# Kernel tuning notes

Hardware: AMD Instinct MI355X
Metric: run time of the kernel (lower is better)

Reference implementation:

```python
import jax, jax.numpy as jnp
import numpy as np
from jax import lax

K = 3
K2 = K * K
EPS = 1e-5


def conv3x3(x, w, b=None):
    # x [B,C,H,W], w [O,C,3,3], padding=1, stride=1
    out = lax.conv_general_dilated(x, w, (1, 1), [(1, 1), (1, 1)],
                                   dimension_numbers=('NCHW', 'OIHW', 'NCHW'))
    if b is not None:
        out = out + b[None, :, None, None]
    return out


def deform_conv(x, w_off, b_off, w_mod, b_mod, w):
    # DCNv2-style deformable conv, k=3, stride=1, pad=1, dilation=1, no bias.
    B, C, H, W = x.shape
    O = w.shape[0]
    off = conv3x3(x, w_off, b_off).reshape(B, K2, 2, H, W)   # (dy,dx) per tap
    mod = 2.0 * jax.nn.sigmoid(conv3x3(x, w_mod, b_mod))      # [B,9,H,W]
    dy, dx = off[:, :, 0], off[:, :, 1]

    ky = (jnp.arange(K) - 1).astype(x.dtype)
    base_y = jnp.repeat(ky, K)   # [9]
    base_x = jnp.tile(ky, K)     # [9]
    ii = jnp.arange(H, dtype=x.dtype)[:, None]
    jj = jnp.arange(W, dtype=x.dtype)[None, :]
    py = ii[None, None] + base_y[None, :, None, None] + dy   # [B,9,H,W]
    px = jj[None, None] + base_x[None, :, None, None] + dx

    def sample(xb, pyb, pxb):
        # xb [C,H,W]; pyb/pxb [9,H,W] -> [C,9,H,W], bilinear w/ zero pad
        y0 = jnp.floor(pyb)
        x0 = jnp.floor(pxb)
        wy = pyb - y0
        wx = pxb - x0
        flat = xb.reshape(C, -1)
        acc = jnp.zeros((C, K2, H, W), xb.dtype)
        for yc, xc, wt in ((y0, x0, (1 - wy) * (1 - wx)),
                           (y0, x0 + 1, (1 - wy) * wx),
                           (y0 + 1, x0, wy * (1 - wx)),
                           (y0 + 1, x0 + 1, wy * wx)):
            yi = yc.astype(jnp.int32)
            xi = xc.astype(jnp.int32)
            valid = (yi >= 0) & (yi < H) & (xi >= 0) & (xi < W)
            idx = (jnp.clip(yi, 0, H - 1) * W + jnp.clip(xi, 0, W - 1)).reshape(-1)
            g = jnp.take(flat, idx, axis=1).reshape(C, K2, H, W)
            acc = acc + g * (wt * valid)[None]
        return acc

    patches = jax.vmap(sample)(x, py, px)          # [B,C,9,H,W]
    patches = patches * mod[:, None]               # modulated
    return jnp.einsum('bckhw,ock->bohw', patches, w.reshape(O, C, K2))


def bn_relu(x):
    # BatchNorm2d(affine=False), train-mode batch stats, biased variance
    mean = jnp.mean(x, axis=(0, 2, 3), keepdims=True)
    var = jnp.mean(jnp.square(x - mean), axis=(0, 2, 3), keepdims=True)
    return jax.nn.relu((x - mean) * lax.rsqrt(var + EPS))


def maxpool2(x):
    return lax.reduce_window(x, -jnp.inf, lax.max, (1, 1, 2, 2), (1, 1, 2, 2), 'VALID')


def setup_inputs() -> dict:
    key = jax.random.key(0)
    ks = jax.random.split(key, 11)
    B, Cin, Cout, H, W = 4, 64, 128, 128, 128
    std1 = 1.0 / np.sqrt(Cin * K2)
    std2 = 1.0 / np.sqrt(Cout * K2)
    return {
        'x': jax.random.normal(ks[0], (B, Cin, H, W), jnp.float32),
        'w_off1': jax.random.normal(ks[1], (2 * K2, Cin, K, K), jnp.float32) * 0.01,
        'b_off1': jax.random.normal(ks[2], (2 * K2,), jnp.float32) * 0.01,
        'w_mod1': jax.random.normal(ks[3], (K2, Cin, K, K), jnp.float32) * 0.01,
        'b_mod1': jnp.zeros((K2,), jnp.float32),
        'w1': jax.random.normal(ks[4], (Cout, Cin, K, K), jnp.float32) * std1,
        'w_off2': jax.random.normal(ks[5], (2 * K2, Cout, K, K), jnp.float32) * 0.01,
        'b_off2': jax.random.normal(ks[6], (2 * K2,), jnp.float32) * 0.01,
        'w_mod2': jax.random.normal(ks[7], (K2, Cout, K, K), jnp.float32) * 0.01,
        'b_mod2': jnp.zeros((K2,), jnp.float32),
        'w2': jax.random.normal(ks[8], (Cout, Cout, K, K), jnp.float32) * std2,
    }


def reference(x, w_off1, b_off1, w_mod1, b_mod1, w1,
              w_off2, b_off2, w_mod2, b_mod2, w2):
    h = bn_relu(deform_conv(x, w_off1, b_off1, w_mod1, b_mod1, w1))
    h = bn_relu(deform_conv(h, w_off2, b_off2, w_mod2, b_mod2, w2))
    return maxpool2(h)
```

## Files before the change

### kernel.cpp

```cpp
#include <hip/hip_runtime.h>
#include <math.h>

#define HH 128
#define WW 128
#define HWSZ 16384

typedef __attribute__((ext_vector_type(8))) _Float16 h8;
typedef __attribute__((ext_vector_type(2))) _Float16 h2;
typedef __attribute__((ext_vector_type(4))) float f32x4;
typedef __attribute__((ext_vector_type(2))) float f32x2;
typedef unsigned short ushort;

__device__ __forceinline__ ushort f2h(float f) {
    _Float16 h = (_Float16)f;
    ushort u;
    __builtin_memcpy(&u, &h, 2);
    return u;
}
__device__ __forceinline__ unsigned f2h2(float lo, float hi) {
    h2 r;
    r.x = (_Float16)lo;
    r.y = (_Float16)hi;
    unsigned u;
    __builtin_memcpy(&u, &r, 4);
    return u;
}
__device__ __forceinline__ f32x2 unpk_h2(unsigned u) {
    h2 h;
    __builtin_memcpy(&h, &u, 4);
    return (f32x2){(float)h.x, (float)h.y};
}

__global__ __launch_bounds__(256) void prep_weights(
    const float* __restrict__ w1, const float* __restrict__ w2,
    const float* __restrict__ w_off1, const float* __restrict__ w_mod1,
    const float* __restrict__ w_off2, const float* __restrict__ w_mod2,
    ushort* __restrict__ Wt1, ushort* __restrict__ Wt2,
    ushort* __restrict__ Wo1, ushort* __restrict__ Wo2) {
    int bid = blockIdx.x, tid = threadIdx.x;
    if (bid < 336) {
        int i = bid * 256 + tid;
        int o = i / 672, kq = i % 672;
        int k = kq / 72, c = kq % 72;
        float v = (k < 9 && c < 64) ? w1[(o * 64 + c) * 9 + k] : 0.f;
        Wt1[i] = f2h(v);
    } else if (bid < 960) {
        int i = (bid - 336) * 256 + tid;
        int o = i / 1248, kq = i % 1248;
        int k = kq / 136, c = kq % 136;
        float v = (k < 9 && c < 128) ? w2[(o * 128 + c) * 9 + k] : 0.f;
        Wt2[i] = f2h(v);
    } else if (bid < 1032) {
        int i = (bid - 960) * 256 + tid;
        int o = i / 576, kap = i % 576;
        int k = kap / 64, c = kap % 64;
        float v = 0.f;
        if (o < 18) v = w_off1[(o * 64 + c) * 9 + k];
        else if (o < 27) v = w_mod1[((o - 18) * 64 + c) * 9 + k];
        Wo1[i] = f2h(v);
    } else {
        int i = (bid - 1032) * 256 + tid;
        int o = i / 1152, kap = i % 1152;
        int k = kap / 128, c = kap % 128;
        float v = 0.f;
        if (o < 18) v = w_off2[(o * 128 + c) * 9 + k];
        else if (o < 27) v = w_mod2[((o - 18) * 128 + c) * 9 + k];
        Wo2[i] = f2h(v);
    }
}

template <int C>
__global__ __launch_bounds__(256) void nhwc_cvt(const float* __restrict__ xin,
                                                unsigned* __restrict__ xout) {
    __shared__ float tile[64][C + 1];
    const int m0 = blockIdx.x * 64;
    const int b = m0 >> 14;
    const int hw0 = m0 & 16383;
    const int t = threadIdx.x;
    const int pr = t & 63, cr = t >> 6;
#pragma unroll
    for (int it = 0; it < C / 4; ++it) {
        int c = it * 4 + cr;
        tile[pr][c] = xin[(((size_t)(b * C + c)) << 14) + hw0 + pr];
    }
    __syncthreads();
    constexpr int CH = C / 2;
#pragma unroll
    for (int it = 0; it < 64 * CH / 256; ++it) {
        int slot = it * 256 + t;
        int p = slot / CH, cc = slot % CH;
        xout[(size_t)(m0 + p) * CH + cc] =
            f2h2(tile[p][2 * cc], tile[p][2 * cc + 1]);
    }
}

__global__ __launch_bounds__(256) void bn_apply_ew(
    const unsigned* __restrict__ xin, const float* __restrict__ praw,
    unsigned* __restrict__ xout) {
    __shared__ float lstats[256];
    if (threadIdx.x < 128) {
        int c = threadIdx.x;
        float s = 0.f, q = 0.f;
#pragma unroll
        for (int r = 0; r < 8; ++r) {
            s += praw[r * 256 + c];
            q += praw[r * 256 + 128 + c];
        }
        float mean = s / 65536.f;
        float var = q / 65536.f - mean * mean;
        lstats[c] = mean;
        lstats[128 + c] = rsqrtf(var + 1e-5f);
    }
    __syncthreads();
    int i = blockIdx.x * 256 + threadIdx.x;
    uint4 v = ((const uint4*)xin)[i];
    int c0 = ((i * 4) & 63) * 2;
    unsigned ov[4];
    unsigned in[4] = {v.x, v.y, v.z, v.w};
#pragma unroll
    for (int d = 0; d < 4; ++d) {
        int c = c0 + 2 * d;
        f32x2 f = unpk_h2(in[d]);
        float a = fmaxf(0.f, (f.x - lstats[c]) * lstats[128 + c]);
        float b2 = fmaxf(0.f, (f.y - lstats[c + 1]) * lstats[128 + c + 1]);
        ov[d] = f2h2(a, b2);
    }
    ((uint4*)xout)[i] = uint4{ov[0], ov[1], ov[2], ov[3]};
}

template <int C>
__global__ __launch_bounds__(256) void offmod_nhwc(
    const ushort* __restrict__ xh, const ushort* __restrict__ wt,
    const float* __restrict__ b_off, const float* __restrict__ b_mod,
    float* __restrict__ dyb, float* __restrict__ dxb, float* __restrict__ mob,
    float* __restrict__ praw) {
    constexpr int K = C * 9;
    if (blockIdx.x < 8) praw[blockIdx.x * 256 + threadIdx.x] = 0.f;
    const int m0 = blockIdx.x * 64;
    const int b = m0 >> 14;
    const int hw0 = m0 & 16383;
    const int h = hw0 >> 7;
    const int w0 = hw0 & 127;
    const int tid = threadIdx.x;
    const int lane = tid & 63, wv = tid >> 6;
    const int n16 = lane & 15, quad = lane >> 4;
    const int p = wv * 16 + n16;
    const int w = w0 + p;

    int tbase[9];
    bool tval[9];
#pragma unroll
    for (int k = 0; k < 9; ++k) {
        int yy = h + k / 3 - 1, xx = w + k % 3 - 1;
        tval[k] = ((unsigned)yy < 128u) && ((unsigned)xx < 128u);
        int cy = min(max(yy, 0), 127), cx = min(max(xx, 0), 127);
        tbase[k] = ((b << 14) + (cy << 7) + cx) * C + quad * 8;
    }

    f32x4 acc[2];
    acc[0] = (f32x4){0.f, 0.f, 0.f, 0.f};
    acc[1] = (f32x4){0.f, 0.f, 0.f, 0.f};

    const ushort* b0p = wt + (size_t)n16 * K + quad * 8;
    const ushort* b1p = wt + (size_t)(16 + n16) * K + quad * 8;

#pragma unroll
    for (int s = 0; s < K / 32; ++s) {
        const int k = (s * 32) / C;
        const int c0 = (s * 32) % C;
        h8 a = {0, 0, 0, 0, 0, 0, 0, 0};
        if (tval[k]) a = *(const h8*)(xh + (size_t)tbase[k] + c0);
        const h8 bv0 = *(const h8*)(b0p + s * 32);
        const h8 bv1 = *(const h8*)(b1p + s * 32);
        acc[0] = __builtin_amdgcn_mfma_f32_16x16x32_f16(a, bv0, acc[0], 0, 0, 0);
        acc[1] = __builtin_amdgcn_mfma_f32_16x16x32_f16(a, bv1, acc[1], 0, 0, 0);
    }

    __shared__ float sm[32 * 65];
#pragma unroll
    for (int nt = 0; nt < 2; ++nt) {
        int n = nt * 16 + n16;
        int pb = wv * 16 + quad * 4;
#pragma unroll
        for (int r = 0; r < 4; ++r) sm[n * 65 + pb + r] = acc[nt][r];
    }
    __syncthreads();
    {
        int n = tid >> 3, i8 = tid & 7;
        if (n < 27) {
            const float* sp = sm + n * 65 + i8 * 8;
            int px = hw0 + i8 * 8;
            if (n < 18) {
                int k = n >> 1;
                float bias = b_off[n];
                float* dst =
                    ((n & 1) ? dxb : dyb) + (((size_t)(b * 9 + k)) << 14) + px;
#pragma unroll
                for (int j = 0; j < 8; j += 4) {
                    float4 v = make_float4(sp[j] + bias, sp[j + 1] + bias,
                                           sp[j + 2] + bias, sp[j + 3] + bias);
                    *(float4*)(dst + j) = v;
                }
            } else {
                float bias = b_mod[n - 18];
                float* dst = mob + (((size_t)(b * 9 + (n - 18))) << 14) + px;
#pragma unroll
                for (int j = 0; j < 8; j += 4) {
                    float4 v;
                    v.x = 2.f / (1.f + expf(-(sp[j] + bias)));
                    v.y = 2.f / (1.f + expf(-(sp[j + 1] + bias)));
                    v.z = 2.f / (1.f + expf(-(sp[j + 2] + bias)));
                    v.w = 2.f / (1.f + expf(-(sp[j + 3] + bias)));
                    *(float4*)(dst + j) = v;
                }
            }
        }
    }
}

template <int C>
__global__ __launch_bounds__(256, 8) void deform_mfma3(
    const ushort* __restrict__ xh, const float* __restrict__ dyb,
    const float* __restrict__ dxb, const float* __restrict__ mob,
    const ushort* __restrict__ wt, unsigned* __restrict__ xout,
    float* __restrict__ praw) {
    constexpr int PIX = 32;
    constexpr int NCH = C / 8;
    constexpr int NCC = C / 8;
    constexpr int NIT = PIX * NCC / 256;
    constexpr int HNIT = (NIT >= 2) ? NIT / 2 : 1;
    constexpr int SH = (C / 32) / 2 > 0 ? (C / 32) / 2 : 1;
    constexpr int CPW = C + 8;
    constexpr int KP = ((9 * CPW + 31) / 32) * 32;
    constexpr int ABUF = PIX * C;
    constexpr int LOOPB = 2 * ABUF * 2 + PIX * 9 * 4 + PIX * 9 * 8;
    constexpr int EPIB = 128 * (PIX + 1) * 4;
    constexpr int SMEMB = LOOPB > EPIB ? LOOPB : EPIB;

    __shared__ __align__(16) char smem_raw[SMEMB];
    ushort* abuf0 = (ushort*)smem_raw;
    ushort* abuf1 = abuf0 + ABUF;
    int* tbl = (int*)(abuf0 + 2 * ABUF);
    unsigned* twl = (unsigned*)(smem_raw + 2 * ABUF * 2 + PIX * 9 * 4);

    const int bid = (blockIdx.x & 7) * (gridDim.x >> 3) + (blockIdx.x >> 3);
    const int m0 = bid * PIX;
    const int b = m0 >> 14;
    const int hw0 = m0 & 16383;
    const int h = hw0 >> 7, w0 = hw0 & 127;
    const int tid = threadIdx.x;
    const int lane = tid & 63, wv = tid >> 6;
    const int n16 = lane & 15, quad = lane >> 4;
    const int xr = n16 & (NCH - 1);

    for (int r = tid; r < PIX * 9; r += 256) {
        int p = r & (PIX - 1), k = r >> 5;
        int oi = ((b * 9 + k) << 14) + hw0 + p;
        float py = (float)(h + k / 3 - 1) + dyb[oi];
        float px = (float)(w0 + p + k % 3 - 1) + dxb[oi];
        float mv = mob[oi];
        float y0f = floorf(py), x0f = floorf(px);
        float wy = py - y0f, wx = px - x0f;
        int y0 = (int)y0f, x0 = (int)x0f;
        int y1 = y0 + 1, x1 = x0 + 1;
        float f00 = (1.f - wy) * (1.f - wx) *
                    (((unsigned)y0 < 128u && (unsigned)x0 < 128u) ? mv : 0.f);
        float f01 = (1.f - wy) * wx *
                    (((unsigned)y0 < 128u && (unsigned)x1 < 128u) ? mv : 0.f);
        float f10 = wy * (1.f - wx) *
                    (((unsigned)y1 < 128u && (unsigned)x0 < 128u) ? mv : 0.f);
        float f11 = wy * wx *
                    (((unsigned)y1 < 128u && (unsigned)x1 < 128u) ? mv : 0.f);
        int cy0 = min(max(y0, 0), 127), cy1 = min(max(y1, 0), 127);
        int cx0 = min(max(x0, 0), 127), cx1 = min(max(x1, 0), 127);
        int base00 = (((b << 14) + (cy0 << 7) + cx0)) * C;
        int flags = ((cy1 != cy0) ? 2 : 0) | ((cx1 != cx0) ? 1 : 0);
        int s = p * 9 + k;
        tbl[s] = base00 | flags;
        twl[2 * s] = f2h2(f00, f01);
        twl[2 * s + 1] = f2h2(f10, f11);
    }
    __syncthreads();

    auto issue_loads = [&](int kc, int it0, uint4 (&q)[HNIT][4],
                           uint2 (&fw)[HNIT]) {
#pragma unroll
        for (int j = 0; j < HNIT; ++j) {
            int e = (it0 + j) * 256 + tid;
            int p = e / NCC, cc = e % NCC;
            int s = p * 9 + kc;
            int ent = tbl[s];
            fw[j] = *(const uint2*)&twl[2 * s];
            int base = ent & ~3;
            int dxo = (ent & 1) ? C : 0;
            int dyo = (ent & 2) ? (C << 7) : 0;
            const ushort* pp = xh + (size_t)base + cc * 8;
            q[j][0] = *(const uint4*)(pp);
            q[j][1] = *(const uint4*)(pp + dxo);
            q[j][2] = *(const uint4*)(pp + dyo);
            q[j][3] = *(const uint4*)(pp + dyo + dxo);
        }
    };
    auto interp_write = [&](ushort* dst, int it0, uint4 (&q)[HNIT][4],
                            uint2 (&fw)[HNIT]) {
#pragma unroll
        for (int j = 0; j < HNIT; ++j) {
            int e = (it0 + j) * 256 + tid;
            int p = e / NCC, cc = e % NCC;
            h2 w01, w23;
            __builtin_memcpy(&w01, &fw[j].x, 4);
            __builtin_memcpy(&w23, &fw[j].y, 4);
            h8 F0 = {w01.x, w01.x, w01.x, w01.x, w01.x, w01.x, w01.x, w01.x};
            h8 F1 = {w01.y, w01.y, w01.y, w01.y, w01.y, w01.y, w01.y, w01.y};
            h8 F2 = {w23.x, w23.x, w23.x, w23.x, w23.x, w23.x, w23.x, w23.x};
            h8 F3 = {w23.y, w23.y, w23.y, w23.y, w23.y, w23.y, w23.y, w23.y};
            h8 a0, a1, a2, a3;
            __builtin_memcpy(&a0, &q[j][0], 16);
            __builtin_memcpy(&a1, &q[j][1], 16);
            __builtin_memcpy(&a2, &q[j][2], 16);
            __builtin_memcpy(&a3, &q[j][3], 16);
            h8 v = a0 * F0 + a1 * F1 + a2 * F2 + a3 * F3;
            uint4 ov;
            __builtin_memcpy(&ov, &v, 16);
            int ccs = cc ^ (p & (NCH - 1));
            *(uint4*)&dst[p * C + ccs * 8] = ov;
        }
    };

    f32x4 acc[2][2];
#pragma unroll
    for (int mt = 0; mt < 2; ++mt)
#pragma unroll
        for (int nt = 0; nt < 2; ++nt) acc[mt][nt] = (f32x4){0.f, 0.f, 0.f, 0.f};

    const ushort* bbase[2];
#pragma unroll
    for (int nt = 0; nt < 2; ++nt)
        bbase[nt] = wt + (size_t)(wv * 32 + nt * 16 + n16) * KP + quad * 8;

    auto mfma_run = [&](const ushort* ab, int kc, int s0, int s1) {
#pragma unroll
        for (int s = s0; s < s1; ++s) {
            h8 av[2], bv[2];
            int ch = (s * 4 + quad) ^ xr;
#pragma unroll
            for (int mt = 0; mt < 2; ++mt)
                av[mt] = *(const h8*)(ab + (mt * 16 + n16) * C + ch * 8);
#pragma unroll
            for (int nt = 0; nt < 2; ++nt)
                bv[nt] = *(const h8*)(bbase[nt] + kc * CPW + s * 32);
#pragma unroll
            for (int mt = 0; mt < 2; ++mt)
#pragma unroll
                for (int nt = 0; nt < 2; ++nt)
                    acc[mt][nt] = __builtin_amdgcn_mfma_f32_16x16x32_f16(
                        av[mt], bv[nt], acc[mt][nt], 0, 0, 0);
        }
    };

    {
        uint4 q[HNIT][4];
        uint2 fw[HNIT];
        issue_loads(0, 0, q, fw);
        interp_write(abuf0, 0, q, fw);
        if constexpr (NIT >= 2) {
            issue_loads(0, HNIT, q, fw);
            interp_write(abuf0, HNIT, q, fw);
        }
    }
    __syncthreads();

#pragma unroll 1
    for (int kc = 0; kc < 9; ++kc) {
        const ushort* ab = (kc & 1) ? abuf1 : abuf0;
        ushort* dst = (kc & 1) ? abuf0 : abuf1;
        uint4 q[HNIT][4];
        uint2 fw[HNIT];
        if (kc < 8) issue_loads(kc + 1, 0, q, fw);
        __builtin_amdgcn_s_setprio(1);
        mfma_run(ab, kc, 0, SH);
        __builtin_amdgcn_s_setprio(0);
        if constexpr (NIT >= 2) {
            if (kc < 8) {
                interp_write(dst, 0, q, fw);
                issue_loads(kc + 1, HNIT, q, fw);
            }
            __builtin_amdgcn_s_setprio(1);
            mfma_run(ab, kc, SH, C / 32);
            __builtin_amdgcn_s_setprio(0);
            if (kc < 8) interp_write(dst, HNIT, q, fw);
        } else {
            __builtin_amdgcn_s_setprio(1);
            mfma_run(ab, kc, SH, C / 32);
            __builtin_amdgcn_s_setprio(0);
            if (kc < 8) interp_write(dst, 0, q, fw);
        }
        __syncthreads();
    }

    float* sm = (float*)smem_raw;
    constexpr int SROW = PIX + 1;
#pragma unroll
    for (int mt = 0; mt < 2; ++mt)
#pragma unroll
        for (int nt = 0; nt < 2; ++nt) {
            int o = wv * 32 + nt * 16 + n16;
            int mb = mt * 16 + quad * 4;
#pragma unroll
            for (int r = 0; r < 4; ++r) sm[o * SROW + mb + r] = acc[mt][nt][r];
        }
    __syncthreads();
    {
        int o = tid >> 1, half = tid & 1;
        const float* sp = sm + o * SROW + half * 16;
        float s = 0.f, qq = 0.f;
#pragma unroll
        for (int i = 0; i < 16; i += 4) {
            float4 v = make_float4(sp[i], sp[i + 1], sp[i + 2], sp[i + 3]);
            s += v.x + v.y + v.z + v.w;
            qq += v.x * v.x + v.y * v.y + v.z * v.z + v.w * v.w;
        }
        s += __shfl_down(s, 1, 64);
        qq += __shfl_down(qq, 1, 64);
        if (half == 0) {
            float* pr = praw + (blockIdx.x & 7) * 256;
            atomicAdd(&pr[o], s);
            atomicAdd(&pr[128 + o], qq);
        }
    }
    {
        int p = tid >> 3, cc8 = tid & 7;
        unsigned ov[8];
#pragma unroll
        for (int j = 0; j < 8; ++j) {
            int c = cc8 * 16 + 2 * j;
            ov[j] = f2h2(sm[c * SROW + p], sm[(c + 1) * SROW + p]);
        }
        uint4* dst = (uint4*)(xout + ((size_t)(m0 + p)) * 64 + cc8 * 8);
        dst[0] = uint4{ov[0], ov[1], ov[2], ov[3]};
        dst[1] = uint4{ov[4], ov[5], ov[6], ov[7]};
    }
}

template <int C>
__global__ __launch_bounds__(256, 8) void deform_mfma3p(
    const ushort* __restrict__ xh, const float* __restrict__ dyb,
    const float* __restrict__ dxb, const float* __restrict__ mob,
    const ushort* __restrict__ wt, float* __restrict__ pout,
    float* __restrict__ praw) {
    constexpr int PIX = 32;
    constexpr int NCH = C / 8;
    constexpr int NCC = C / 8;
    constexpr int NIT = PIX * NCC / 256;
    constexpr int HNIT = (NIT >= 2) ? NIT / 2 : 1;
    constexpr int SH = (C / 32) / 2 > 0 ? (C / 32) / 2 : 1;
    constexpr int CPW = C + 8;
    constexpr int KP = ((9 * CPW + 31) / 32) * 32;
    constexpr int ABUF = PIX * C;
    constexpr int LOOPB = 2 * ABUF * 2 + PIX * 9 * 4 + PIX * 9 * 8;
    constexpr int EPIB = 128 * (PIX + 1) * 4;
    constexpr int SMEMB = LOOPB > EPIB ? LOOPB : EPIB;

    __shared__ __align__(16) char smem_raw[SMEMB];
    ushort* abuf0 = (ushort*)smem_raw;
    ushort* abuf1 = abuf0 + ABUF;
    int* tbl = (int*)(abuf0 + 2 * ABUF);
    unsigned* twl = (unsigned*)(smem_raw + 2 * ABUF * 2 + PIX * 9 * 4);

    const int bid = (blockIdx.x & 7) * (gridDim.x >> 3) + (blockIdx.x >> 3);
    const int b = bid >> 9;
    const int rp = (bid >> 3) & 63;
    const int g = bid & 7;
    const int tid = threadIdx.x;
    const int lane = tid & 63, wv = tid >> 6;
    const int n16 = lane & 15, quad = lane >> 4;
    const int xr = n16 & (NCH - 1);

    for (int r = tid; r < PIX * 9; r += 256) {
        int p = r & (PIX - 1), k = r >> 5;
        int row = 2 * rp + (p >> 4), col = g * 16 + (p & 15);
        int oi = ((b * 9 + k) << 14) + (row << 7) + col;
        float py = (float)(row + k / 3 - 1) + dyb[oi];
        float px = (float)(col + k % 3 - 1) + dxb[oi];
        float mv = mob[oi];
        float y0f = floorf(py), x0f = floorf(px);
        float wy = py - y0f, wx = px - x0f;
        int y0 = (int)y0f, x0 = (int)x0f;
        int y1 = y0 + 1, x1 = x0 + 1;
        float f00 = (1.f - wy) * (1.f - wx) *
                    (((unsigned)y0 < 128u && (unsigned)x0 < 128u) ? mv : 0.f);
        float f01 = (1.f - wy) * wx *
                    (((unsigned)y0 < 128u && (unsigned)x1 < 128u) ? mv : 0.f);
        float f10 = wy * (1.f - wx) *
                    (((unsigned)y1 < 128u && (unsigned)x0 < 128u) ? mv : 0.f);
        float f11 = wy * wx *
                    (((unsigned)y1 < 128u && (unsigned)x1 < 128u) ? mv : 0.f);
        int cy0 = min(max(y0, 0), 127), cy1 = min(max(y1, 0), 127);
        int cx0 = min(max(x0, 0), 127), cx1 = min(max(x1, 0), 127);
        int base00 = (((b << 14) + (cy0 << 7) + cx0)) * C;
        int flags = ((cy1 != cy0) ? 2 : 0) | ((cx1 != cx0) ? 1 : 0);
        int s = p * 9 + k;
        tbl[s] = base00 | flags;
        twl[2 * s] = f2h2(f00, f01);
        twl[2 * s + 1] = f2h2(f10, f11);
    }
    __syncthreads();

    auto issue_loads = [&](int kc, int it0, uint4 (&q)[HNIT][4],
                           uint2 (&fw)[HNIT]) {
#pragma unroll
        for (int j = 0; j < HNIT; ++j) {
            int e = (it0 + j) * 256 + tid;
            int p = e / NCC, cc = e % NCC;
            int s = p * 9 + kc;
            int ent = tbl[s];
            fw[j] = *(const uint2*)&twl[2 * s];
            int base = ent & ~3;
            int dxo = (ent & 1) ? C : 0;
            int dyo = (ent & 2) ? (C << 7) : 0;
            const ushort* pp = xh + (size_t)base + cc * 8;
            q[j][0] = *(const uint4*)(pp);
            q[j][1] = *(const uint4*)(pp + dxo);
            q[j][2] = *(const uint4*)(pp + dyo);
            q[j][3] = *(const uint4*)(pp + dyo + dxo);
        }
    };
    auto interp_write = [&](ushort* dst, int it0, uint4 (&q)[HNIT][4],
                            uint2 (&fw)[HNIT]) {
#pragma unroll
        for (int j = 0; j < HNIT; ++j) {
            int e = (it0 + j) * 256 + tid;
            int p = e / NCC, cc = e % NCC;
            h2 w01, w23;
            __builtin_memcpy(&w01, &fw[j].x, 4);
            __builtin_memcpy(&w23, &fw[j].y, 4);
            h8 F0 = {w01.x, w01.x, w01.x, w01.x, w01.x, w01.x, w01.x, w01.x};
            h8 F1 = {w01.y, w01.y, w01.y, w01.y, w01.y, w01.y, w01.y, w01.y};
            h8 F2 = {w23.x, w23.x, w23.x, w23.x, w23.x, w23.x, w23.x, w23.x};
            h8 F3 = {w23.y, w23.y, w23.y, w23.y, w23.y, w23.y, w23.y, w23.y};
            h8 a0, a1, a2, a3;
            __builtin_memcpy(&a0, &q[j][0], 16);
            __builtin_memcpy(&a1, &q[j][1], 16);
            __builtin_memcpy(&a2, &q[j][2], 16);
            __builtin_memcpy(&a3, &q[j][3], 16);
            h8 v = a0 * F0 + a1 * F1 + a2 * F2 + a3 * F3;
            uint4 ov;
            __builtin_memcpy(&ov, &v, 16);
            int ccs = cc ^ (p & (NCH - 1));
            *(uint4*)&dst[p * C + ccs * 8] = ov;
        }
    };

    f32x4 acc[2][2];
#pragma unroll
    for (int mt = 0; mt < 2; ++mt)
#pragma unroll
        for (int nt = 0; nt < 2; ++nt) acc[mt][nt] = (f32x4){0.f, 0.f, 0.f, 0.f};

    const ushort* bbase[2];
#pragma unroll
    for (int nt = 0; nt < 2; ++nt)
        bbase[nt] = wt + (size_t)(wv * 32 + nt * 16 + n16) * KP + quad * 8;

    auto mfma_run = [&](const ushort* ab, int kc, int s0, int s1) {
#pragma unroll
        for (int s = s0; s < s1; ++s) {
            h8 av[2], bv[2];
            int ch = (s * 4 + quad) ^ xr;
#pragma unroll
            for (int mt = 0; mt < 2; ++mt)
                av[mt] = *(const h8*)(ab + (mt * 16 + n16) * C + ch * 8);
#pragma unroll
            for (int nt = 0; nt < 2; ++nt)
                bv[nt] = *(const h8*)(bbase[nt] + kc * CPW + s * 32);
#pragma unroll
            for (int mt = 0; mt < 2; ++mt)
#pragma unroll
                for (int nt = 0; nt < 2; ++nt)
                    acc[mt][nt] = __builtin_amdgcn_mfma_f32_16x16x32_f16(
                        av[mt], bv[nt], acc[mt][nt], 0, 0, 0);
        }
    };

    {
        uint4 q[HNIT][4];
        uint2 fw[HNIT];
        issue_loads(0, 0, q, fw);
        interp_write(abuf0, 0, q, fw);
        if constexpr (NIT >= 2) {
            issue_loads(0, HNIT, q, fw);
            interp_write(abuf0, HNIT, q, fw);
        }
    }
    __syncthreads();

#pragma unroll 1
    for (int kc = 0; kc < 9; ++kc) {
        const ushort* ab = (kc & 1) ? abuf1 : abuf0;
        ushort* dst = (kc & 1) ? abuf0 : abuf1;
        uint4 q[HNIT][4];
        uint2 fw[HNIT];
        if (kc < 8) issue_loads(kc + 1, 0, q, fw);
        __builtin_amdgcn_s_setprio(1);
        mfma_run(ab, kc, 0, SH);
        __builtin_amdgcn_s_setprio(0);
        if constexpr (NIT >= 2) {
            if (kc < 8) {
                interp_write(dst, 0, q, fw);
                issue_loads(kc + 1, HNIT, q, fw);
            }
            __builtin_amdgcn_s_setprio(1);
            mfma_run(ab, kc, SH, C / 32);
            __builtin_amdgcn_s_setprio(0);
            if (kc < 8) interp_write(dst, HNIT, q, fw);
        } else {
            __builtin_amdgcn_s_setprio(1);
            mfma_run(ab, kc, SH, C / 32);
            __builtin_amdgcn_s_setprio(0);
            if (kc < 8) interp_write(dst, 0, q, fw);
        }
        __syncthreads();
    }

    float* sm = (float*)smem_raw;
    constexpr int SROW = PIX + 1;
#pragma unroll
    for (int mt = 0; mt < 2; ++mt)
#pragma unroll
        for (int nt = 0; nt < 2; ++nt) {
            int o = wv * 32 + nt * 16 + n16;
            int mb = mt * 16 + quad * 4;
#pragma unroll
            for (int r = 0; r < 4; ++r) sm[o * SROW + mb + r] = acc[mt][nt][r];
        }
    __syncthreads();
    {
        int o = tid >> 1, half = tid & 1;
        const float* so = sm + o * SROW;
        const float* sp = so + half * 16;
        float s = 0.f, qq = 0.f;
#pragma unroll
        for (int i = 0; i < 16; i += 4) {
            float4 v = make_float4(sp[i], sp[i + 1], sp[i + 2], sp[i + 3]);
            s += v.x + v.y + v.z + v.w;
            qq += v.x * v.x + v.y * v.y + v.z * v.z + v.w * v.w;
        }
        s += __shfl_down(s, 1, 64);
        qq += __shfl_down(qq, 1, 64);
        if (half == 0) {
            float* pr = praw + (blockIdx.x & 7) * 256;
            atomicAdd(&pr[o], s);
            atomicAdd(&pr[128 + o], qq);
        }
        float4 pv;
#pragma unroll
        for (int i = 0; i < 4; ++i) {
            int pc = half * 4 + i;
            float m0v = fmaxf(so[2 * pc], so[2 * pc + 1]);
            float m1v = fmaxf(so[16 + 2 * pc], so[16 + 2 * pc + 1]);
            ((float*)&pv)[i] = fmaxf(m0v, m1v);
        }
        *(float4*)(pout + (((size_t)(b * 128 + o)) << 12) + rp * 64 + g * 8 +
                   half * 4) = pv;
    }
}

__global__ __launch_bounds__(256) void pool_norm(const float* __restrict__ pout,
                                                 const float* __restrict__ praw,
                                                 float* __restrict__ out) {
    __shared__ float lstats[256];
    if (threadIdx.x < 128) {
        int c = threadIdx.x;
        float s = 0.f, q = 0.f;
#pragma unroll
        for (int r = 0; r < 8; ++r) {
            s += praw[r * 256 + c];
            q += praw[r * 256 + 128 + c];
        }
        float mean = s / 65536.f;
        float var = q / 65536.f - mean * mean;
        lstats[c] = mean;
        lstats[128 + c] = rsqrtf(var + 1e-5f);
    }
    __syncthreads();
    int i = blockIdx.x * 256 + threadIdx.x;
    int c = (i >> 10) & 127;
    float mean = lstats[c], rstd = lstats[128 + c];
    float4 v = ((const float4*)pout)[i];
    v.x = fmaxf(0.f, (v.x - mean) * rstd);
    v.y = fmaxf(0.f, (v.y - mean) * rstd);
    v.z = fmaxf(0.f, (v.z - mean) * rstd);
    v.w = fmaxf(0.f, (v.w - mean) * rstd);
    ((float4*)out)[i] = v;
}

extern "C" void kernel_launch(void* const* d_in, const int* in_sizes, int n_in,
                              void* d_out, int out_size, void* d_ws,
                              size_t ws_size, hipStream_t stream) {
    (void)in_sizes;
    (void)n_in;
    (void)out_size;
    (void)ws_size;
    const float* x = (const float*)d_in[0];
    const float* w_off1 = (const float*)d_in[1];
    const float* b_off1 = (const float*)d_in[2];
    const float* w_mod1 = (const float*)d_in[3];
    const float* b_mod1 = (const float*)d_in[4];
    const float* w1 = (const float*)d_in[5];
    const float* w_off2 = (const float*)d_in[6];
    const float* b_off2 = (const float*)d_in[7];
    const float* w_mod2 = (const float*)d_in[8];
    const float* b_mod2 = (const float*)d_in[9];
    const float* w2 = (const float*)d_in[10];
    float* out = (float*)d_out;
    float* ws = (float*)d_ws;

    ushort* Wt1 = (ushort*)ws;
    ushort* Wt2 = (ushort*)(ws + 43008);
    ushort* Wo1 = (ushort*)(ws + 43008 + 79872);
    ushort* Wo2 = (ushort*)(ws + 43008 + 79872 + 16384);
    float* dyb = ws + 172032;
    float* dxb = dyb + 589824;
    float* mob = dxb + 589824;
    float* hbuf = mob + 589824;
    float* xhf = hbuf + 8388608;
    float* h1hf = xhf + 2097152;
    float* praw = h1hf + 4194304;
    ushort* xh = (ushort*)xhf;
    ushort* h1h = (ushort*)h1hf;

    prep_weights<<<1176, 256, 0, stream>>>(w1, w2, w_off1, w_mod1, w_off2,
                                           w_mod2, Wt1, Wt2, Wo1, Wo2);

    nhwc_cvt<64><<<1024, 256, 0, stream>>>(x, (unsigned*)xh);
    offmod_nhwc<64><<<1024, 256, 0, stream>>>(xh, Wo1, b_off1, b_mod1, dyb, dxb,
                                              mob, praw);
    deform_mfma3<64><<<2048, 256, 0, stream>>>(xh, dyb, dxb, mob, Wt1,
                                               (unsigned*)hbuf, praw);
    bn_apply_ew<<<4096, 256, 0, stream>>>((const unsigned*)hbuf, praw,
                                          (unsigned*)h1h);

    offmod_nhwc<128><<<1024, 256, 0, stream>>>(h1h, Wo2, b_off2, b_mod2, dyb,
                                               dxb, mob, praw);
    deform_mfma3p<128><<<2048, 256, 0, stream>>>(h1h, dyb, dxb, mob, Wt2, hbuf,
                                                 praw);
    pool_norm<<<2048, 256, 0, stream>>>(hbuf, praw, out);
}
```

Before: 299.4 us.

## Compute BN stats and maxpool from MFMA registers, drop LDS epilogue staging

The final deformable-conv kernel no longer stages the accumulator tile through shared memory for its epilogue. The per-channel sum and sum-of-squares come from registers with cross-lane xor shuffles, and the 2x2 maxpool is taken directly from the MFMA output layout. This removes an LDS round trip and a barrier and shrinks the shared-memory footprint to the main-loop buffers. The launch-bounds occupancy hint on both deform kernels is also lowered from 8 to 6, giving the compiler more registers at some cost in waves per CU; pooled outputs are now written as scalar stores rather than float4.

```diff
diff --git a/kernel.cpp b/kernel.cpp
--- a/kernel.cpp
+++ b/kernel.cpp
@@ -219,7 +219,7 @@
 }
 
 template <int C>
-__global__ __launch_bounds__(256, 8) void deform_mfma3(
+__global__ __launch_bounds__(256, 6) void deform_mfma3(
     const ushort* __restrict__ xh, const float* __restrict__ dyb,
     const float* __restrict__ dxb, const float* __restrict__ mob,
     const ushort* __restrict__ wt, unsigned* __restrict__ xout,
@@ -443,7 +443,7 @@
 }
 
 template <int C>
-__global__ __launch_bounds__(256, 8) void deform_mfma3p(
+__global__ __launch_bounds__(256, 6) void deform_mfma3p(
     const ushort* __restrict__ xh, const float* __restrict__ dyb,
     const float* __restrict__ dxb, const float* __restrict__ mob,
     const ushort* __restrict__ wt, float* __restrict__ pout,
@@ -457,9 +457,7 @@
     constexpr int CPW = C + 8;
     constexpr int KP = ((9 * CPW + 31) / 32) * 32;
     constexpr int ABUF = PIX * C;
-    constexpr int LOOPB = 2 * ABUF * 2 + PIX * 9 * 4 + PIX * 9 * 8;
-    constexpr int EPIB = 128 * (PIX + 1) * 4;
-    constexpr int SMEMB = LOOPB > EPIB ? LOOPB : EPIB;
+    constexpr int SMEMB = 2 * ABUF * 2 + PIX * 9 * 4 + PIX * 9 * 8;
 
     __shared__ __align__(16) char smem_raw[SMEMB];
     ushort* abuf0 = (ushort*)smem_raw;
@@ -622,46 +620,35 @@
         __syncthreads();
     }
 
-    float* sm = (float*)smem_raw;
-    constexpr int SROW = PIX + 1;
-#pragma unroll
-    for (int mt = 0; mt < 2; ++mt)
-#pragma unroll
-        for (int nt = 0; nt < 2; ++nt) {
-            int o = wv * 32 + nt * 16 + n16;
-            int mb = mt * 16 + quad * 4;
-#pragma unroll
-            for (int r = 0; r < 4; ++r) sm[o * SROW + mb + r] = acc[mt][nt][r];
-        }
-    __syncthreads();
-    {
-        int o = tid >> 1, half = tid & 1;
-        const float* so = sm + o * SROW;
-        const float* sp = so + half * 16;
+#pragma unroll
+    for (int nt = 0; nt < 2; ++nt) {
+        int o = wv * 32 + nt * 16 + n16;
         float s = 0.f, qq = 0.f;
 #pragma unroll
-        for (int i = 0; i < 16; i += 4) {
-            float4 v = make_float4(sp[i], sp[i + 1], sp[i + 2], sp[i + 3]);
-            s += v.x + v.y + v.z + v.w;
-            qq += v.x * v.x + v.y * v.y + v.z * v.z + v.w * v.w;
-        }
-        s += __shfl_down(s, 1, 64);
-        qq += __shfl_down(qq, 1, 64);
-        if (half == 0) {
+        for (int mt = 0; mt < 2; ++mt)
+#pragma unroll
+            for (int r = 0; r < 4; ++r) {
+                float v = acc[mt][nt][r];
+                s += v;
+                qq += v * v;
+            }
+        s += __shfl_xor(s, 16, 64);
+        s += __shfl_xor(s, 32, 64);
+        qq += __shfl_xor(qq, 16, 64);
+        qq += __shfl_xor(qq, 32, 64);
+        if (quad == 0) {
             float* pr = praw + (blockIdx.x & 7) * 256;
             atomicAdd(&pr[o], s);
             atomicAdd(&pr[128 + o], qq);
         }
-        float4 pv;
-#pragma unroll
-        for (int i = 0; i < 4; ++i) {
-            int pc = half * 4 + i;
-            float m0v = fmaxf(so[2 * pc], so[2 * pc + 1]);
-            float m1v = fmaxf(so[16 + 2 * pc], so[16 + 2 * pc + 1]);
-            ((float*)&pv)[i] = fmaxf(m0v, m1v);
-        }
-        *(float4*)(pout + (((size_t)(b * 128 + o)) << 12) + rp * 64 + g * 8 +
-                   half * 4) = pv;
+        float* po = pout + (((size_t)(b * 128 + o)) << 12) + rp * 64 + g * 8;
+#pragma unroll
+        for (int rp2 = 0; rp2 < 2; ++rp2) {
+            float m =
+                fmaxf(fmaxf(acc[0][nt][2 * rp2], acc[0][nt][2 * rp2 + 1]),
+                      fmaxf(acc[1][nt][2 * rp2], acc[1][nt][2 * rp2 + 1]));
+            po[quad * 2 + rp2] = m;
+        }
     }
 }
 
```

Result: faster. 289.7 us (-3.3%).
